# Kernel tuning notes

Hardware: AMD Instinct MI355X
Metric: run time of the kernel (lower is better)

The kernel has to match this reference:

```python
import jax, jax.numpy as jnp
import numpy as np


def to_float8(x, exp_bits=4, mant_bits=3):
    # Faithful port of the torch to_float8: clamp exponent, round mantissa.
    max_exp = 2 ** (exp_bits - 1) - 1
    scale = 2.0 ** mant_bits
    sign = jnp.sign(x)
    xa = jnp.abs(x)
    e = jnp.clip(jnp.floor(jnp.log2(xa + 1e-08)), -max_exp, max_exp)
    p = jnp.exp2(e)
    mant_q = jnp.round((xa / p - 1.0) * scale) / scale
    return sign * (1.0 + mant_q) * p


def setup_inputs() -> dict:
    key = jax.random.key(0)
    k0, k1, k2, k3, k4 = jax.random.split(key, 5)
    Bz, Din, L, N, Dout = 32, 512, 512, 512, 512
    u = jax.random.normal(k0, (Bz, Din, L), jnp.float32)
    # |A| < 1 for a stable length-512 recurrence
    A_diag = jax.random.uniform(k1, (N,), jnp.float32, 0.0, 0.9)
    B = jax.random.normal(k2, (N, Din), jnp.float32) * (1.0 / np.sqrt(Din))
    C = jax.random.normal(k3, (Dout, N), jnp.float32) * (1.0 / np.sqrt(N))
    D = jax.random.normal(k4, (Dout, Din), jnp.float32) * (1.0 / np.sqrt(Din))
    return {"u": u, "A_diag": A_diag, "B": B, "C": C, "D": D}


def reference(u, A_diag, B, C, D):
    int_bits, mant_bits = 4, 3
    q = lambda t: to_float8(t, int_bits, mant_bits)
    A_q = q(A_diag)[None, :]          # [1, N]
    B_q, C_q, D_q = q(B), q(C), q(D)
    Bt = B_q.T                         # [Din, N]
    # row_checksum(B_q.t()): append column of row sums -> constant across steps
    right_cs = jnp.concatenate([Bt, Bt.sum(axis=1, keepdims=True)], axis=1)  # [Din, N+1]
    Bz, Din, L = u.shape
    N = A_diag.shape[0]
    u_t = jnp.transpose(u, (2, 0, 1))  # [L, Bz, Din]

    def step(state, ut):
        # col_checksum(ut): append row of column sums
        left_cs = jnp.concatenate([ut, ut.sum(axis=0, keepdims=True)], axis=0)  # [Bz+1, Din]
        prod_cs = left_cs @ right_cs                 # [Bz+1, N+1] checksum-padded matmul
        right_term = prod_cs[:-1, :-1]               # ut @ B_q.T  (ABFT mask is discarded in forward)
        state_q = q(state * A_q + right_term)        # [Bz, N]
        y = q(state_q @ C_q.T + ut @ D_q.T)          # [Bz, Dout]
        return state_q, y

    state0 = jnp.zeros((Bz, N), u.dtype)
    _, Y = jax.lax.scan(step, state0, u_t)           # [L, Bz, Dout]
    return jnp.transpose(Y, (1, 2, 0))               # [Bz, Dout, L]
```

## Files before the change

kernel.cpp:

```cpp
#include <hip/hip_runtime.h>


#define DINX 512
#define LSEQ 512
#define NDIM 512

__device__ __forceinline__ float q8(float x) {
    float xa = fabsf(x);
    float w  = __fadd_rn(xa, 1e-8f);
    int e = (int)((__float_as_uint(w) >> 23) & 0xFFu) - 127;
    e = e < -7 ? -7 : (e > 7 ? 7 : e);
    float p    = __int_as_float((unsigned)((e + 127) << 23));
    float invp = __int_as_float((unsigned)((127 - e) << 23));
    float t  = __fmul_rn(__fsub_rn(__fmul_rn(xa, invp), 1.0f), 8.0f);
    float m  = __fmul_rn(rintf(t), 0.125f);
    float r  = __fmul_rn(__fadd_rn(1.0f, m), p);
    return copysignf(r, x);
}

__global__ __launch_bounds__(256) void quantBA(const float* __restrict__ B,
                                               const float* __restrict__ A,
                                               float* __restrict__ Bqt,
                                               float* __restrict__ Aq) {
    __shared__ float tl[32][33];
    if (blockIdx.x == 0 && blockIdx.y == 0) {
        Aq[threadIdx.x]       = q8(A[threadIdx.x]);
        Aq[256 + threadIdx.x] = q8(A[256 + threadIdx.x]);
    }
    const int r0 = blockIdx.y * 32, c0 = blockIdx.x * 32;
    const int x = threadIdx.x & 31, y = threadIdx.x >> 5;
#pragma unroll
    for (int i = 0; i < 32; i += 8)
        tl[y + i][x] = q8(B[(r0 + y + i) * 512 + c0 + x]);
    __syncthreads();
#pragma unroll
    for (int i = 0; i < 32; i += 8)
        Bqt[(c0 + y + i) * 512 + r0 + x] = tl[x][y + i];
}

__device__ __forceinline__ void gemm_pass(const float* __restrict__ X,
                                          const float* __restrict__ W,
                                          int m0, int n0, int KTOT,
                                          float (&acc)[2][4][2][4],
                                          float (*Xs)[128], float (*Ws)[128],
                                          int tid) {
    const int tx = tid & 15, ty = tid >> 4;
    const int srow = tid >> 4, sseg4 = (tid & 15) * 4;
    const float* xp = X + (size_t)srow * 512 + m0 + sseg4;
    const float* wp = W + (size_t)srow * 512 + n0 + sseg4;
    for (int k0 = 0; k0 < KTOT; k0 += 32) {
        float4 x0 = *(const float4*)xp;
        float4 x1 = *(const float4*)(xp + 64);
        float4 x2 = *(const float4*)(xp + 16 * 512);
        float4 x3 = *(const float4*)(xp + 16 * 512 + 64);
        float4 w0 = *(const float4*)wp;
        float4 w1 = *(const float4*)(wp + 64);
        float4 w2 = *(const float4*)(wp + 16 * 512);
        float4 w3 = *(const float4*)(wp + 16 * 512 + 64);
        xp += 32 * 512; wp += 32 * 512;
        __syncthreads();
        *(float4*)&Xs[srow][sseg4]           = x0;
        *(float4*)&Xs[srow][64 + sseg4]      = x1;
        *(float4*)&Xs[16 + srow][sseg4]      = x2;
        *(float4*)&Xs[16 + srow][64 + sseg4] = x3;
        *(float4*)&Ws[srow][sseg4]           = w0;
        *(float4*)&Ws[srow][64 + sseg4]      = w1;
        *(float4*)&Ws[16 + srow][sseg4]      = w2;
        *(float4*)&Ws[16 + srow][64 + sseg4] = w3;
        __syncthreads();
#pragma unroll
        for (int k = 0; k < 32; ++k) {
            float a[2][4], b[2][4];
            *(float4*)&a[0][0] = *(const float4*)&Xs[k][tx * 4];
            *(float4*)&a[1][0] = *(const float4*)&Xs[k][64 + tx * 4];
            *(float4*)&b[0][0] = *(const float4*)&Ws[k][ty * 4];
            *(float4*)&b[1][0] = *(const float4*)&Ws[k][64 + ty * 4];
#pragma unroll
            for (int p = 0; p < 2; ++p)
#pragma unroll
                for (int i = 0; i < 4; ++i)
#pragma unroll
                    for (int q = 0; q < 2; ++q)
#pragma unroll
                        for (int j = 0; j < 4; ++j)
                            acc[p][i][q][j] = fmaf(a[p][i], b[q][j], acc[p][i][q][j]);
        }
    }
}

__global__ __launch_bounds__(256, 4) void fused_RqCD(const float* __restrict__ u,
                                                     const float* __restrict__ Bqt,
                                                     const float* __restrict__ C,
                                                     const float* __restrict__ D,
                                                     float* __restrict__ R,
                                                     float* __restrict__ Cqt,
                                                     float* __restrict__ Dqt) {
    __shared__ float ldsbuf[2 * 32 * 128];
    const int zz = blockIdx.x;
    const int tid = threadIdx.x;
    if (zz < 512) {
        float (*Xs)[128] = (float(*)[128])ldsbuf;
        float (*Ws)[128] = (float(*)[128])(ldsbuf + 32 * 128);
        const int b = zz & 31, t0 = ((zz >> 5) & 3) * 128, n0 = (zz >> 7) * 128;
        const int tx = tid & 15, ty = tid >> 4;
        const float* ub = u + (size_t)b * (DINX * LSEQ);
        float acc[2][4][2][4] = {};
        gemm_pass(ub, Bqt, t0, n0, DINX, acc, Xs, Ws, tid);
        float* Rb = R + (size_t)b * (LSEQ * NDIM);
#pragma unroll
        for (int p = 0; p < 2; ++p)
#pragma unroll
            for (int i = 0; i < 4; ++i) {
                float* row = Rb + (size_t)(t0 + p * 64 + tx * 4 + i) * NDIM + n0;
                *(float4*)(row + ty * 4)      = make_float4(acc[p][i][0][0], acc[p][i][0][1],
                                                            acc[p][i][0][2], acc[p][i][0][3]);
                *(float4*)(row + 64 + ty * 4) = make_float4(acc[p][i][1][0], acc[p][i][1][1],
                                                            acc[p][i][1][2], acc[p][i][1][3]);
            }
    } else {
        float (*tl)[33] = (float(*)[33])ldsbuf;
        const int d = zz - 512;
        const float* in = (d >> 8) ? D : C;
        float* out      = (d >> 8) ? Dqt : Cqt;
        const int c0 = (d & 15) * 32, r0 = ((d >> 4) & 15) * 32;
        const int x = tid & 31, y = tid >> 5;
#pragma unroll
        for (int i = 0; i < 32; i += 8)
            tl[y + i][x] = q8(in[(r0 + y + i) * 512 + c0 + x]);
        __syncthreads();
#pragma unroll
        for (int i = 0; i < 32; i += 8)
            out[(c0 + y + i) * 512 + r0 + x] = tl[x][y + i];
    }
}

__global__ __launch_bounds__(256, 3) void fused_Drec(const float* __restrict__ u,
                                                     const float* __restrict__ Dqt,
                                                     const float* __restrict__ R,
                                                     const float* __restrict__ Aq,
                                                     float* __restrict__ Pd,
                                                     float* __restrict__ S) {
    __shared__ float ldsbuf[2 * 32 * 128];
    const int zz = blockIdx.x;
    const int tid = threadIdx.x;
    if (zz >= 256) {
        float (*Xs)[128] = (float(*)[128])ldsbuf;
        float (*Ws)[128] = (float(*)[128])(ldsbuf + 32 * 128);
        const int d = zz - 256;
        const int b = d & 31, t0 = ((d >> 5) & 3) * 128, o0 = (d >> 7) * 128;
        const int tx = tid & 15, ty = tid >> 4;
        const float* ub = u + (size_t)b * (DINX * LSEQ);
        float acc[2][4][2][4] = {};
        gemm_pass(ub, Dqt, t0, o0, DINX, acc, Xs, Ws, tid);
        float* Yb = Pd + (size_t)b * (NDIM * LSEQ);
#pragma unroll
        for (int q = 0; q < 2; ++q)
#pragma unroll
            for (int j = 0; j < 4; ++j) {
                float* row = Yb + (size_t)(o0 + q * 64 + ty * 4 + j) * LSEQ + t0;
                *(float4*)(row + tx * 4)      = make_float4(acc[0][0][q][j], acc[0][1][q][j],
                                                            acc[0][2][q][j], acc[0][3][q][j]);
                *(float4*)(row + 64 + tx * 4) = make_float4(acc[1][0][q][j], acc[1][1][q][j],
                                                            acc[1][2][q][j], acc[1][3][q][j]);
            }
    } else {
        float (*tile)[68] = (float(*)[68])ldsbuf;
        const int b  = zz >> 3;
        const int n0 = (zz & 7) * 64;
        const int n  = tid & 63;
        const bool act = tid < 64;
        float a = 0.0f, s = 0.0f;
        const float* Rb = R + (size_t)b * (LSEQ * NDIM) + n0;
        float* Sb = S + (size_t)b * (NDIM * LSEQ) + (size_t)n0 * LSEQ;
        if (act) a = Aq[n0 + n];
        const int c = (n & 3) * 4;
        const int rbase = n >> 2;
        for (int t0 = 0; t0 < LSEQ; t0 += 16) {
            if (act) {
#pragma unroll
                for (int tt = 0; tt < 16; ++tt) {
                    float r = Rb[(size_t)(t0 + tt) * NDIM + n];
                    s = q8(__fadd_rn(__fmul_rn(s, a), r));
                    tile[tt][n] = s;
                }
            }
            __syncthreads();
            if (act) {
#pragma unroll
                for (int p = 0; p < 4; ++p) {
                    int row = p * 16 + rbase;
                    float4 v = make_float4(tile[c + 0][row], tile[c + 1][row],
                                           tile[c + 2][row], tile[c + 3][row]);
                    *(float4*)(Sb + (size_t)row * LSEQ + t0 + c) = v;
                }
            }
            __syncthreads();
        }
    }
}

__global__ __launch_bounds__(256) void gemm_YC(const float* __restrict__ S,
                                               const float* __restrict__ Cqt,
                                               float* __restrict__ Y) {
    __shared__ float Xs[32][128];
    __shared__ float Ws[32][128];
    const int b  = blockIdx.z;
    const int t0 = blockIdx.x * 128, o0 = blockIdx.y * 128;
    const int tid = threadIdx.x;
    const int tx = tid & 15, ty = tid >> 4;
    const float* Sb = S + (size_t)b * (NDIM * LSEQ);
    float acc[2][4][2][4] = {};
    gemm_pass(Sb, Cqt, t0, o0, NDIM, acc, Xs, Ws, tid);

    float* Yb = Y + (size_t)b * (NDIM * LSEQ);
#pragma unroll
    for (int q = 0; q < 2; ++q)
#pragma unroll
        for (int j = 0; j < 4; ++j) {
            float* row = Yb + (size_t)(o0 + q * 64 + ty * 4 + j) * LSEQ + t0;
            float4 v0 = *(const float4*)(row + tx * 4);
            float4 v1 = *(const float4*)(row + 64 + tx * 4);
            *(float4*)(row + tx * 4) =
                make_float4(q8(__fadd_rn(acc[0][0][q][j], v0.x)),
                            q8(__fadd_rn(acc[0][1][q][j], v0.y)),
                            q8(__fadd_rn(acc[0][2][q][j], v0.z)),
                            q8(__fadd_rn(acc[0][3][q][j], v0.w)));
            *(float4*)(row + 64 + tx * 4) =
                make_float4(q8(__fadd_rn(acc[1][0][q][j], v1.x)),
                            q8(__fadd_rn(acc[1][1][q][j], v1.y)),
                            q8(__fadd_rn(acc[1][2][q][j], v1.z)),
                            q8(__fadd_rn(acc[1][3][q][j], v1.w)));
        }
}

extern "C" void kernel_launch(void* const* d_in, const int* in_sizes, int n_in,
                              void* d_out, int out_size, void* d_ws, size_t ws_size,
                              hipStream_t stream) {
    const float* u = (const float*)d_in[0];
    const float* A = (const float*)d_in[1];
    const float* B = (const float*)d_in[2];
    const float* C = (const float*)d_in[3];
    const float* D = (const float*)d_in[4];

    float* ws  = (float*)d_ws;
    float* Aq  = ws;
    float* Bqt = Aq + 512;
    float* Cqt = Bqt + 262144;
    float* Dqt = Cqt + 262144;
    float* R   = Dqt + 262144;
    float* S   = R + 8388608;
    float* Y   = (float*)d_out;

    quantBA<<<dim3(16, 16), 256, 0, stream>>>(B, A, Bqt, Aq);
    fused_RqCD<<<1024, 256, 0, stream>>>(u, Bqt, C, D, R, Cqt, Dqt);
    fused_Drec<<<768, 256, 0, stream>>>(u, Dqt, R, Aq, Y, S);
    gemm_YC<<<dim3(4, 4, 32), 256, 0, stream>>>(S, Cqt, Y);
}
```

Before: 372.8 us.

## Load GEMM weight tiles through scalar registers instead of shared memory

The shared GEMM core now reads the weight (B/C/D) tiles with wave-uniform s_load_dwordx16 into SGPRs, so each wave computes a 128x32 output slab. Each lane owns one row pair and uses the scalar weights as broadcast FMA operands. This drops the LDS staging and LDS reads for the weight operand and halves shared memory use, but every k-step now waits on scalar-cache latency, and the epilogue stores become strided per-column writes. gemm_YC is also relaunched as a flat 1D grid with a raised occupancy hint.

Result: slower. 687.8 us (+84.5%).

```diff
diff --git a/kernel.cpp b/kernel.cpp
--- a/kernel.cpp
+++ b/kernel.cpp
@@ -4,6 +4,8 @@
 #define DINX 512
 #define LSEQ 512
 #define NDIM 512
+
+typedef float sf16 __attribute__((ext_vector_type(16)));
 
 __device__ __forceinline__ float q8(float x) {
     float xa = fabsf(x);
@@ -38,53 +40,64 @@
         Bqt[(c0 + y + i) * 512 + r0 + x] = tl[x][y + i];
 }
 
-__device__ __forceinline__ void gemm_pass(const float* __restrict__ X,
+__device__ __forceinline__ void gemm_core(const float* __restrict__ X,
                                           const float* __restrict__ W,
-                                          int m0, int n0, int KTOT,
-                                          float (&acc)[2][4][2][4],
-                                          float (*Xs)[128], float (*Ws)[128],
-                                          int tid) {
-    const int tx = tid & 15, ty = tid >> 4;
+                                          int m0, int n0,
+                                          float (&acc0)[32], float (&acc1)[32],
+                                          float (*Xs)[128], int tid) {
     const int srow = tid >> 4, sseg4 = (tid & 15) * 4;
+    const int l = tid & 63;
+    const int wv = __builtin_amdgcn_readfirstlane(tid >> 6);
     const float* xp = X + (size_t)srow * 512 + m0 + sseg4;
-    const float* wp = W + (size_t)srow * 512 + n0 + sseg4;
-    for (int k0 = 0; k0 < KTOT; k0 += 32) {
+    const float* wp = W + n0 + wv * 32;
+    for (int k0 = 0; k0 < 512; k0 += 32) {
         float4 x0 = *(const float4*)xp;
         float4 x1 = *(const float4*)(xp + 64);
         float4 x2 = *(const float4*)(xp + 16 * 512);
         float4 x3 = *(const float4*)(xp + 16 * 512 + 64);
-        float4 w0 = *(const float4*)wp;
-        float4 w1 = *(const float4*)(wp + 64);
-        float4 w2 = *(const float4*)(wp + 16 * 512);
-        float4 w3 = *(const float4*)(wp + 16 * 512 + 64);
-        xp += 32 * 512; wp += 32 * 512;
+        xp += 32 * 512;
         __syncthreads();
         *(float4*)&Xs[srow][sseg4]           = x0;
         *(float4*)&Xs[srow][64 + sseg4]      = x1;
         *(float4*)&Xs[16 + srow][sseg4]      = x2;
         *(float4*)&Xs[16 + srow][64 + sseg4] = x3;
-        *(float4*)&Ws[srow][sseg4]           = w0;
-        *(float4*)&Ws[srow][64 + sseg4]      = w1;
-        *(float4*)&Ws[16 + srow][sseg4]      = w2;
-        *(float4*)&Ws[16 + srow][64 + sseg4] = w3;
         __syncthreads();
 #pragma unroll
-        for (int k = 0; k < 32; ++k) {
-            float a[2][4], b[2][4];
-            *(float4*)&a[0][0] = *(const float4*)&Xs[k][tx * 4];
-            *(float4*)&a[1][0] = *(const float4*)&Xs[k][64 + tx * 4];
-            *(float4*)&b[0][0] = *(const float4*)&Ws[k][ty * 4];
-            *(float4*)&b[1][0] = *(const float4*)&Ws[k][64 + ty * 4];
-#pragma unroll
-            for (int p = 0; p < 2; ++p)
-#pragma unroll
-                for (int i = 0; i < 4; ++i)
-#pragma unroll
-                    for (int q = 0; q < 2; ++q)
-#pragma unroll
-                        for (int j = 0; j < 4; ++j)
-                            acc[p][i][q][j] = fmaf(a[p][i], b[q][j], acc[p][i][q][j]);
-        }
+        for (int g = 0; g < 16; ++g) {
+            sf16 b0, b1, b2, b3;
+            asm volatile("s_load_dwordx16 %0, %1, %2" : "=s"(b0) : "s"(wp), "i"(g * 4096));
+            asm volatile("s_load_dwordx16 %0, %1, %2" : "=s"(b1) : "s"(wp), "i"(g * 4096 + 64));
+            asm volatile("s_load_dwordx16 %0, %1, %2" : "=s"(b2) : "s"(wp), "i"(g * 4096 + 2048));
+            asm volatile("s_load_dwordx16 %0, %1, %2" : "=s"(b3) : "s"(wp), "i"(g * 4096 + 2112));
+            float a00 = Xs[2 * g][l];
+            float a01 = Xs[2 * g][64 + l];
+            float a10 = Xs[2 * g + 1][l];
+            float a11 = Xs[2 * g + 1][64 + l];
+            asm volatile("s_waitcnt lgkmcnt(0)"
+                         : "+s"(b0), "+s"(b1), "+s"(b2), "+s"(b3));
+#pragma unroll
+            for (int j = 0; j < 16; ++j) {
+                acc0[j] = fmaf(a00, b0[j], acc0[j]);
+                acc1[j] = fmaf(a01, b0[j], acc1[j]);
+            }
+#pragma unroll
+            for (int j = 0; j < 16; ++j) {
+                acc0[16 + j] = fmaf(a00, b1[j], acc0[16 + j]);
+                acc1[16 + j] = fmaf(a01, b1[j], acc1[16 + j]);
+            }
+#pragma unroll
+            for (int j = 0; j < 16; ++j) {
+                acc0[j] = fmaf(a10, b2[j], acc0[j]);
+                acc1[j] = fmaf(a11, b2[j], acc1[j]);
+            }
+#pragma unroll
+            for (int j = 0; j < 16; ++j) {
+                acc0[16 + j] = fmaf(a10, b3[j], acc0[16 + j]);
+                acc1[16 + j] = fmaf(a11, b3[j], acc1[16 + j]);
+            }
+            __builtin_amdgcn_sched_barrier(0);
+        }
+        wp += 32 * 512;
     }
 }
 
@@ -95,28 +108,27 @@
                                                      float* __restrict__ R,
                                                      float* __restrict__ Cqt,
                                                      float* __restrict__ Dqt) {
-    __shared__ float ldsbuf[2 * 32 * 128];
+    __shared__ float ldsbuf[32 * 128];
     const int zz = blockIdx.x;
     const int tid = threadIdx.x;
     if (zz < 512) {
         float (*Xs)[128] = (float(*)[128])ldsbuf;
-        float (*Ws)[128] = (float(*)[128])(ldsbuf + 32 * 128);
         const int b = zz & 31, t0 = ((zz >> 5) & 3) * 128, n0 = (zz >> 7) * 128;
-        const int tx = tid & 15, ty = tid >> 4;
         const float* ub = u + (size_t)b * (DINX * LSEQ);
-        float acc[2][4][2][4] = {};
-        gemm_pass(ub, Bqt, t0, n0, DINX, acc, Xs, Ws, tid);
-        float* Rb = R + (size_t)b * (LSEQ * NDIM);
-#pragma unroll
-        for (int p = 0; p < 2; ++p)
-#pragma unroll
-            for (int i = 0; i < 4; ++i) {
-                float* row = Rb + (size_t)(t0 + p * 64 + tx * 4 + i) * NDIM + n0;
-                *(float4*)(row + ty * 4)      = make_float4(acc[p][i][0][0], acc[p][i][0][1],
-                                                            acc[p][i][0][2], acc[p][i][0][3]);
-                *(float4*)(row + 64 + ty * 4) = make_float4(acc[p][i][1][0], acc[p][i][1][1],
-                                                            acc[p][i][1][2], acc[p][i][1][3]);
-            }
+        float acc0[32] = {}, acc1[32] = {};
+        gemm_core(ub, Bqt, t0, n0, acc0, acc1, Xs, tid);
+        const int l = tid & 63;
+        const int wv = tid >> 6;
+        const int c0 = n0 + wv * 32;
+        float* r0 = R + (size_t)b * (LSEQ * NDIM) + (size_t)(t0 + l) * NDIM + c0;
+        float* r1 = r0 + (size_t)64 * NDIM;
+#pragma unroll
+        for (int j4 = 0; j4 < 8; ++j4) {
+            *(float4*)(r0 + j4 * 4) = make_float4(acc0[j4 * 4], acc0[j4 * 4 + 1],
+                                                  acc0[j4 * 4 + 2], acc0[j4 * 4 + 3]);
+            *(float4*)(r1 + j4 * 4) = make_float4(acc1[j4 * 4], acc1[j4 * 4 + 1],
+                                                  acc1[j4 * 4 + 2], acc1[j4 * 4 + 3]);
+        }
     } else {
         float (*tl)[33] = (float(*)[33])ldsbuf;
         const int d = zz - 512;
@@ -140,29 +152,25 @@
                                                      const float* __restrict__ Aq,
                                                      float* __restrict__ Pd,
                                                      float* __restrict__ S) {
-    __shared__ float ldsbuf[2 * 32 * 128];
+    __shared__ float ldsbuf[32 * 128];
     const int zz = blockIdx.x;
     const int tid = threadIdx.x;
     if (zz >= 256) {
         float (*Xs)[128] = (float(*)[128])ldsbuf;
-        float (*Ws)[128] = (float(*)[128])(ldsbuf + 32 * 128);
         const int d = zz - 256;
         const int b = d & 31, t0 = ((d >> 5) & 3) * 128, o0 = (d >> 7) * 128;
-        const int tx = tid & 15, ty = tid >> 4;
         const float* ub = u + (size_t)b * (DINX * LSEQ);
-        float acc[2][4][2][4] = {};
-        gemm_pass(ub, Dqt, t0, o0, DINX, acc, Xs, Ws, tid);
+        float acc0[32] = {}, acc1[32] = {};
+        gemm_core(ub, Dqt, t0, o0, acc0, acc1, Xs, tid);
+        const int l = tid & 63;
+        const int wv = tid >> 6;
+        const int c0 = o0 + wv * 32;
         float* Yb = Pd + (size_t)b * (NDIM * LSEQ);
 #pragma unroll
-        for (int q = 0; q < 2; ++q)
-#pragma unroll
-            for (int j = 0; j < 4; ++j) {
-                float* row = Yb + (size_t)(o0 + q * 64 + ty * 4 + j) * LSEQ + t0;
-                *(float4*)(row + tx * 4)      = make_float4(acc[0][0][q][j], acc[0][1][q][j],
-                                                            acc[0][2][q][j], acc[0][3][q][j]);
-                *(float4*)(row + 64 + tx * 4) = make_float4(acc[1][0][q][j], acc[1][1][q][j],
-                                                            acc[1][2][q][j], acc[1][3][q][j]);
-            }
+        for (int j = 0; j < 32; ++j) {
+            Yb[(size_t)(c0 + j) * LSEQ + t0 + l]      = acc0[j];
+            Yb[(size_t)(c0 + j) * LSEQ + t0 + 64 + l] = acc1[j];
+        }
     } else {
         float (*tile)[68] = (float(*)[68])ldsbuf;
         const int b  = zz >> 3;
@@ -199,38 +207,27 @@
     }
 }
 
-__global__ __launch_bounds__(256) void gemm_YC(const float* __restrict__ S,
-                                               const float* __restrict__ Cqt,
-                                               float* __restrict__ Y) {
+__global__ __launch_bounds__(256, 2) void gemm_YC(const float* __restrict__ S,
+                                                  const float* __restrict__ Cqt,
+                                                  float* __restrict__ Y) {
     __shared__ float Xs[32][128];
-    __shared__ float Ws[32][128];
-    const int b  = blockIdx.z;
-    const int t0 = blockIdx.x * 128, o0 = blockIdx.y * 128;
+    const int zz = blockIdx.x;
     const int tid = threadIdx.x;
-    const int tx = tid & 15, ty = tid >> 4;
+    const int b = zz & 31, t0 = ((zz >> 5) & 3) * 128, o0 = (zz >> 7) * 128;
     const float* Sb = S + (size_t)b * (NDIM * LSEQ);
-    float acc[2][4][2][4] = {};
-    gemm_pass(Sb, Cqt, t0, o0, NDIM, acc, Xs, Ws, tid);
-
+    float acc0[32] = {}, acc1[32] = {};
+    gemm_core(Sb, Cqt, t0, o0, acc0, acc1, Xs, tid);
+    const int l = tid & 63;
+    const int wv = tid >> 6;
+    const int c0 = o0 + wv * 32;
     float* Yb = Y + (size_t)b * (NDIM * LSEQ);
 #pragma unroll
-    for (int q = 0; q < 2; ++q)
-#pragma unroll
-        for (int j = 0; j < 4; ++j) {
-            float* row = Yb + (size_t)(o0 + q * 64 + ty * 4 + j) * LSEQ + t0;
-            float4 v0 = *(const float4*)(row + tx * 4);
-            float4 v1 = *(const float4*)(row + 64 + tx * 4);
-            *(float4*)(row + tx * 4) =
-                make_float4(q8(__fadd_rn(acc[0][0][q][j], v0.x)),
-                            q8(__fadd_rn(acc[0][1][q][j], v0.y)),
-                            q8(__fadd_rn(acc[0][2][q][j], v0.z)),
-                            q8(__fadd_rn(acc[0][3][q][j], v0.w)));
-            *(float4*)(row + 64 + tx * 4) =
-                make_float4(q8(__fadd_rn(acc[1][0][q][j], v1.x)),
-                            q8(__fadd_rn(acc[1][1][q][j], v1.y)),
-                            q8(__fadd_rn(acc[1][2][q][j], v1.z)),
-                            q8(__fadd_rn(acc[1][3][q][j], v1.w)));
-        }
+    for (int j = 0; j < 32; ++j) {
+        float* p0 = Yb + (size_t)(c0 + j) * LSEQ + t0 + l;
+        float* p1 = p0 + 64;
+        *p0 = q8(__fadd_rn(acc0[j], *p0));
+        *p1 = q8(__fadd_rn(acc1[j], *p1));
+    }
 }
 
 extern "C" void kernel_launch(void* const* d_in, const int* in_sizes, int n_in,
@@ -254,5 +251,5 @@
     quantBA<<<dim3(16, 16), 256, 0, stream>>>(B, A, Bqt, Aq);
     fused_RqCD<<<1024, 256, 0, stream>>>(u, Bqt, C, D, R, Cqt, Dqt);
     fused_Drec<<<768, 256, 0, stream>>>(u, Dqt, R, Aq, Y, S);
-    gemm_YC<<<dim3(4, 4, 32), 256, 0, stream>>>(S, Cqt, Y);
-}
+    gemm_YC<<<512, 256, 0, stream>>>(S, Cqt, Y);
+}
```

## Double-buffer LDS tiles in D and C GEMM passes to overlap loads

Applied to the files above, without the earlier changes.

Adds a double-buffered GEMM pass that prefetches the next 32-row K tile into registers while computing on the current LDS buffer, so only one barrier is needed per K step. The D-projection part of fused_Drec and gemm_YC switch to it, with LDS doubled to 64 rows per operand and launch bounds lowered to 2 blocks per CU. The aim is to hide global load latency behind FMA work. The cost is more LDS and registers per block, which lowers occupancy and could also slow the recurrence branch that shares fused_Drec.

After: 388.7 us. 4.3% more time.

```diff
diff --git a/kernel.cpp b/kernel.cpp
--- a/kernel.cpp
+++ b/kernel.cpp
@@ -88,6 +88,85 @@
     }
 }
 
+__device__ __forceinline__ void compute32(const float (*Xs)[128], const float (*Ws)[128],
+                                          int base, int tx, int ty,
+                                          float (&acc)[2][4][2][4]) {
+#pragma unroll 2
+    for (int k = 0; k < 32; ++k) {
+        float a[2][4], b[2][4];
+        *(float4*)&a[0][0] = *(const float4*)&Xs[base + k][tx * 4];
+        *(float4*)&a[1][0] = *(const float4*)&Xs[base + k][64 + tx * 4];
+        *(float4*)&b[0][0] = *(const float4*)&Ws[base + k][ty * 4];
+        *(float4*)&b[1][0] = *(const float4*)&Ws[base + k][64 + ty * 4];
+#pragma unroll
+        for (int p = 0; p < 2; ++p)
+#pragma unroll
+            for (int i = 0; i < 4; ++i)
+#pragma unroll
+                for (int q = 0; q < 2; ++q)
+#pragma unroll
+                    for (int j = 0; j < 4; ++j)
+                        acc[p][i][q][j] = fmaf(a[p][i], b[q][j], acc[p][i][q][j]);
+    }
+}
+
+__device__ __forceinline__ void gemm_pass_db(const float* __restrict__ X,
+                                             const float* __restrict__ W,
+                                             int m0, int n0, int KTOT,
+                                             float (&acc)[2][4][2][4],
+                                             float (*Xs)[128], float (*Ws)[128],
+                                             int tid) {
+    const int tx = tid & 15, ty = tid >> 4;
+    const int srow = tid >> 4, sseg4 = (tid & 15) * 4;
+    const float* xp = X + (size_t)srow * 512 + m0 + sseg4;
+    const float* wp = W + (size_t)srow * 512 + n0 + sseg4;
+    {
+        float4 x0 = *(const float4*)xp;
+        float4 x1 = *(const float4*)(xp + 64);
+        float4 x2 = *(const float4*)(xp + 16 * 512);
+        float4 x3 = *(const float4*)(xp + 16 * 512 + 64);
+        float4 w0 = *(const float4*)wp;
+        float4 w1 = *(const float4*)(wp + 64);
+        float4 w2 = *(const float4*)(wp + 16 * 512);
+        float4 w3 = *(const float4*)(wp + 16 * 512 + 64);
+        xp += 32 * 512; wp += 32 * 512;
+        *(float4*)&Xs[srow][sseg4]           = x0;
+        *(float4*)&Xs[srow][64 + sseg4]      = x1;
+        *(float4*)&Xs[16 + srow][sseg4]      = x2;
+        *(float4*)&Xs[16 + srow][64 + sseg4] = x3;
+        *(float4*)&Ws[srow][sseg4]           = w0;
+        *(float4*)&Ws[srow][64 + sseg4]      = w1;
+        *(float4*)&Ws[16 + srow][sseg4]      = w2;
+        *(float4*)&Ws[16 + srow][64 + sseg4] = w3;
+        __syncthreads();
+    }
+    const int NT = KTOT >> 5;
+    for (int it = 0; it < NT - 1; ++it) {
+        const int cb = (it & 1) << 5;
+        const int nb = cb ^ 32;
+        float4 x0 = *(const float4*)xp;
+        float4 x1 = *(const float4*)(xp + 64);
+        float4 x2 = *(const float4*)(xp + 16 * 512);
+        float4 x3 = *(const float4*)(xp + 16 * 512 + 64);
+        float4 w0 = *(const float4*)wp;
+        float4 w1 = *(const float4*)(wp + 64);
+        float4 w2 = *(const float4*)(wp + 16 * 512);
+        float4 w3 = *(const float4*)(wp + 16 * 512 + 64);
+        xp += 32 * 512; wp += 32 * 512;
+        compute32(Xs, Ws, cb, tx, ty, acc);
+        *(float4*)&Xs[nb + srow][sseg4]           = x0;
+        *(float4*)&Xs[nb + srow][64 + sseg4]      = x1;
+        *(float4*)&Xs[nb + 16 + srow][sseg4]      = x2;
+        *(float4*)&Xs[nb + 16 + srow][64 + sseg4] = x3;
+        *(float4*)&Ws[nb + srow][sseg4]           = w0;
+        *(float4*)&Ws[nb + srow][64 + sseg4]      = w1;
+        *(float4*)&Ws[nb + 16 + srow][sseg4]      = w2;
+        *(float4*)&Ws[nb + 16 + srow][64 + sseg4] = w3;
+        __syncthreads();
+    }
+    compute32(Xs, Ws, ((NT - 1) & 1) << 5, tx, ty, acc);
+}
+
 __global__ __launch_bounds__(256, 4) void fused_RqCD(const float* __restrict__ u,
                                                      const float* __restrict__ Bqt,
                                                      const float* __restrict__ C,
@@ -134,24 +213,24 @@
     }
 }
 
-__global__ __launch_bounds__(256, 3) void fused_Drec(const float* __restrict__ u,
+__global__ __launch_bounds__(256, 2) void fused_Drec(const float* __restrict__ u,
                                                      const float* __restrict__ Dqt,
                                                      const float* __restrict__ R,
                                                      const float* __restrict__ Aq,
                                                      float* __restrict__ Pd,
                                                      float* __restrict__ S) {
-    __shared__ float ldsbuf[2 * 32 * 128];
+    __shared__ float ldsbuf[2 * 64 * 128];
     const int zz = blockIdx.x;
     const int tid = threadIdx.x;
     if (zz >= 256) {
         float (*Xs)[128] = (float(*)[128])ldsbuf;
-        float (*Ws)[128] = (float(*)[128])(ldsbuf + 32 * 128);
+        float (*Ws)[128] = (float(*)[128])(ldsbuf + 64 * 128);
         const int d = zz - 256;
         const int b = d & 31, t0 = ((d >> 5) & 3) * 128, o0 = (d >> 7) * 128;
         const int tx = tid & 15, ty = tid >> 4;
         const float* ub = u + (size_t)b * (DINX * LSEQ);
         float acc[2][4][2][4] = {};
-        gemm_pass(ub, Dqt, t0, o0, DINX, acc, Xs, Ws, tid);
+        gemm_pass_db(ub, Dqt, t0, o0, DINX, acc, Xs, Ws, tid);
         float* Yb = Pd + (size_t)b * (NDIM * LSEQ);
 #pragma unroll
         for (int q = 0; q < 2; ++q)
@@ -199,18 +278,18 @@
     }
 }
 
-__global__ __launch_bounds__(256) void gemm_YC(const float* __restrict__ S,
-                                               const float* __restrict__ Cqt,
-                                               float* __restrict__ Y) {
-    __shared__ float Xs[32][128];
-    __shared__ float Ws[32][128];
+__global__ __launch_bounds__(256, 2) void gemm_YC(const float* __restrict__ S,
+                                                  const float* __restrict__ Cqt,
+                                                  float* __restrict__ Y) {
+    __shared__ float Xs[64][128];
+    __shared__ float Ws[64][128];
     const int b  = blockIdx.z;
     const int t0 = blockIdx.x * 128, o0 = blockIdx.y * 128;
     const int tid = threadIdx.x;
     const int tx = tid & 15, ty = tid >> 4;
     const float* Sb = S + (size_t)b * (NDIM * LSEQ);
     float acc[2][4][2][4] = {};
-    gemm_pass(Sb, Cqt, t0, o0, NDIM, acc, Xs, Ws, tid);
+    gemm_pass_db(Sb, Cqt, t0, o0, NDIM, acc, Xs, Ws, tid);
 
     float* Yb = Y + (size_t)b * (NDIM * LSEQ);
 #pragma unroll
```
